# Kernel tuning notes

Measured on AMD Instinct MI355X. Metric: run time of the kernel, lower is better.

## Reference

```python
import jax, jax.numpy as jnp
import numpy as np

BATCH, IN, OUT = 4096, 4096, 4096

def setup_inputs() -> dict:
    key = jax.random.key(0)
    kx, kw, kb = jax.random.split(key, 3)
    x = jax.random.normal(kx, (BATCH, IN), dtype=jnp.float32)
    weights = jax.random.normal(kw, (OUT, IN), dtype=jnp.float32)
    beta = jax.random.normal(kb, (1,), dtype=jnp.float32)
    return {"x": x, "weights": weights, "beta": beta}

def reference(x, weights, beta):
    # original: sum over input dim of broadcast multiply == x @ W^T
    row_sum = jnp.einsum('bi,oi->bo', x, weights)  # [batch, output]
    return jax.nn.relu(1.0 - beta + row_sum)
```

## Files before the change

### kernel.cpp

```cpp
#include <hip/hip_runtime.h>
#include <hip/hip_bf16.h>
#include <cstdint>
#include <cstddef>

#define MDIM 4096
#define NDIM 4096
#define KDIM 4096

#define BM 128
#define BN 128
#define BK 64

typedef __bf16 bf16_t;
typedef bf16_t bf16x8 __attribute__((ext_vector_type(8)));
typedef float f32x4 __attribute__((ext_vector_type(4)));

#define GLDS16(gsrc, ldst)                                                   \
    __builtin_amdgcn_global_load_lds(                                        \
        (__attribute__((address_space(1))) void*)(gsrc),                     \
        (__attribute__((address_space(3))) void*)(ldst), 16, 0, 0)

__global__ void cvt_f32_to_bf16(const float* __restrict__ src,
                                bf16_t* __restrict__ dst, int n) {
    int idx = (blockIdx.x * blockDim.x + threadIdx.x) * 8;
    int stride = gridDim.x * blockDim.x * 8;
    for (int i = idx; i < n; i += stride) {
        const float4* s = reinterpret_cast<const float4*>(src + i);
        float4 a = s[0];
        float4 b = s[1];
        bf16x8 o;
        o[0] = (bf16_t)a.x; o[1] = (bf16_t)a.y;
        o[2] = (bf16_t)a.z; o[3] = (bf16_t)a.w;
        o[4] = (bf16_t)b.x; o[5] = (bf16_t)b.y;
        o[6] = (bf16_t)b.z; o[7] = (bf16_t)b.w;
        *reinterpret_cast<bf16x8*>(dst + i) = o;
    }
}

__global__ void gemm_bt_bf16(const bf16_t* __restrict__ A,
                             const bf16_t* __restrict__ B,
                             const float* __restrict__ beta,
                             float* __restrict__ out) {
    __shared__ __align__(16) bf16_t sA[BM * BK];
    __shared__ __align__(16) bf16_t sB[BN * BK];

    const int tid  = threadIdx.x;
    const int wid  = tid >> 6;
    const int lane = tid & 63;
    const int wr   = wid >> 1;
    const int wc   = wid & 1;
    const int lrow = lane & 15;
    const int kgrp = lane >> 4;

    const int brow = blockIdx.y * BM;
    const int bcol = blockIdx.x * BN;

    f32x4 acc[4][4];
#pragma unroll
    for (int i = 0; i < 4; ++i)
#pragma unroll
        for (int j = 0; j < 4; ++j)
            acc[i][j] = (f32x4){0.f, 0.f, 0.f, 0.f};

    const bf16_t* gA = A + (size_t)brow * KDIM;
    const bf16_t* gB = B + (size_t)bcol * KDIM;

    for (int kt = 0; kt < KDIM; kt += BK) {
#pragma unroll
        for (int i = 0; i < 4; ++i) {
            int g   = i * 256 + tid;
            int row = g >> 3;
            int col = (g & 7) << 3;
            GLDS16(gA + (size_t)row * KDIM + kt + col, sA + g * 8);
            GLDS16(gB + (size_t)row * KDIM + kt + col, sB + g * 8);
        }
        __syncthreads();

#pragma unroll
        for (int ko = 0; ko < 2; ++ko) {
            bf16x8 av[4], bv[4];
#pragma unroll
            for (int mi = 0; mi < 4; ++mi)
                av[mi] = *reinterpret_cast<const bf16x8*>(
                    &sA[(wr * 64 + mi * 16 + lrow) * BK + ko * 32 + kgrp * 8]);
#pragma unroll
            for (int ni = 0; ni < 4; ++ni)
                bv[ni] = *reinterpret_cast<const bf16x8*>(
                    &sB[(wc * 64 + ni * 16 + lrow) * BK + ko * 32 + kgrp * 8]);
#pragma unroll
            for (int mi = 0; mi < 4; ++mi)
#pragma unroll
                for (int ni = 0; ni < 4; ++ni)
                    acc[mi][ni] = __builtin_amdgcn_mfma_f32_16x16x32_bf16(
                        av[mi], bv[ni], acc[mi][ni], 0, 0, 0);
        }
        __syncthreads();
    }

    const float bias = 1.0f - beta[0];
    float* outp = out + (size_t)(brow + wr * 64) * NDIM + bcol + wc * 64;
#pragma unroll
    for (int mi = 0; mi < 4; ++mi) {
#pragma unroll
        for (int ni = 0; ni < 4; ++ni) {
#pragma unroll
            for (int j = 0; j < 4; ++j) {
                int r = mi * 16 + kgrp * 4 + j;
                int c = ni * 16 + lrow;
                float v = acc[mi][ni][j] + bias;
                outp[(size_t)r * NDIM + c] = fmaxf(v, 0.0f);
            }
        }
    }
}

__global__ void gemm_f32_fallback(const float* __restrict__ A,
                                  const float* __restrict__ B,
                                  const float* __restrict__ beta,
                                  float* __restrict__ out) {
    __shared__ float sA[16][17];
    __shared__ float sB[16][17];
    const int tx = threadIdx.x, ty = threadIdx.y;
    const int m = blockIdx.y * 16 + ty;
    const int n = blockIdx.x * 16 + tx;
    float acc = 0.f;
    for (int k0 = 0; k0 < KDIM; k0 += 16) {
        sA[ty][tx] = A[(size_t)m * KDIM + k0 + tx];
        sB[ty][tx] = B[(size_t)(blockIdx.x * 16 + ty) * KDIM + k0 + tx];
        __syncthreads();
#pragma unroll
        for (int k = 0; k < 16; ++k)
            acc += sA[ty][k] * sB[tx][k];
        __syncthreads();
    }
    float v = acc + 1.0f - beta[0];
    out[(size_t)m * NDIM + n] = fmaxf(v, 0.f);
}

extern "C" void kernel_launch(void* const* d_in, const int* in_sizes, int n_in,
                              void* d_out, int out_size, void* d_ws, size_t ws_size,
                              hipStream_t stream) {
    const float* x    = (const float*)d_in[0];
    const float* w    = (const float*)d_in[1];
    const float* beta = (const float*)d_in[2];
    float* out        = (float*)d_out;

    const size_t nelem = (size_t)MDIM * (size_t)KDIM;
    const size_t need  = 2 * nelem * sizeof(bf16_t);

    if (ws_size >= need) {
        bf16_t* xb = (bf16_t*)d_ws;
        bf16_t* wb = xb + nelem;
        cvt_f32_to_bf16<<<2048, 256, 0, stream>>>(x, xb, (int)nelem);
        cvt_f32_to_bf16<<<2048, 256, 0, stream>>>(w, wb, (int)nelem);
        dim3 grid(NDIM / BN, MDIM / BM);
        gemm_bt_bf16<<<grid, 256, 0, stream>>>(xb, wb, beta, out);
    } else {
        dim3 grid(NDIM / 16, MDIM / 16);
        gemm_f32_fallback<<<grid, dim3(16, 16), 0, stream>>>(x, w, beta, out);
    }
}
```

Before: 179.1 us.

## Rewrite bf16 GEMM as 256x256 double-buffered pipelined kernel with swizzled LDS

Replaces the 128x128 single-buffered GEMM with a 256x256-tile, 512-thread kernel that uses 128KB of dynamic LDS, double-buffered across K steps. Global-to-LDS loads for future tiles are interleaved with four MFMA quadrants per iteration, using fine-grained vmcnt waits, barriers and setprio. The LDS layout is XOR-swizzled to reduce bank conflicts, and block IDs are remapped for L2 locality. The aim is to hide memory latency and raise MFMA utilisation. In exchange it brings heavy register pressure, a grid of only 256 blocks (one per CU), and a complex synchronisation scheme that is easy to get wrong.

```diff
diff --git a/kernel.cpp b/kernel.cpp
--- a/kernel.cpp
+++ b/kernel.cpp
@@ -7,9 +7,10 @@
 #define NDIM 4096
 #define KDIM 4096
 
-#define BM 128
-#define BN 128
+#define BM 256
+#define BN 256
 #define BK 64
+#define NT (KDIM / BK)
 
 typedef __bf16 bf16_t;
 typedef bf16_t bf16x8 __attribute__((ext_vector_type(8)));
@@ -19,6 +20,13 @@
     __builtin_amdgcn_global_load_lds(                                        \
         (__attribute__((address_space(1))) void*)(gsrc),                     \
         (__attribute__((address_space(3))) void*)(ldst), 16, 0, 0)
+
+#define BAR()   __builtin_amdgcn_s_barrier()
+#define LGKM0() asm volatile("s_waitcnt lgkmcnt(0)" ::: "memory")
+#define VM4()   asm volatile("s_waitcnt vmcnt(4)" ::: "memory")
+#define VM0()   asm volatile("s_waitcnt vmcnt(0)" ::: "memory")
+
+__device__ __forceinline__ int swz(int q) { return q ^ (((q >> 9) & 1) << 5); }
 
 __global__ void cvt_f32_to_bf16(const float* __restrict__ src,
                                 bf16_t* __restrict__ dst, int n) {
@@ -37,81 +45,140 @@
     }
 }
 
-__global__ void gemm_bt_bf16(const bf16_t* __restrict__ A,
-                             const bf16_t* __restrict__ B,
-                             const float* __restrict__ beta,
-                             float* __restrict__ out) {
-    __shared__ __align__(16) bf16_t sA[BM * BK];
-    __shared__ __align__(16) bf16_t sB[BN * BK];
-
-    const int tid  = threadIdx.x;
-    const int wid  = tid >> 6;
-    const int lane = tid & 63;
-    const int wr   = wid >> 1;
-    const int wc   = wid & 1;
-    const int lrow = lane & 15;
-    const int kgrp = lane >> 4;
-
-    const int brow = blockIdx.y * BM;
-    const int bcol = blockIdx.x * BN;
-
-    f32x4 acc[4][4];
-#pragma unroll
-    for (int i = 0; i < 4; ++i)
+
+#define LOAD_A_HALF(MH, BUF) do {                                            \
+  _Pragma("unroll") for (int mi = 0; mi < 4; ++mi)                           \
+  _Pragma("unroll") for (int ko = 0; ko < 2; ++ko)                           \
+    av[mi][ko] = *(const bf16x8*)(ldsb + ((BUF) << 16) + a_off[(MH)*4 + mi][ko]); \
+} while (0)
+
+#define LOAD_B_PAIR(NH, BUF) do {                                            \
+  _Pragma("unroll") for (int ni = 0; ni < 2; ++ni)                           \
+  _Pragma("unroll") for (int ko = 0; ko < 2; ++ko)                           \
+    bv[(NH)*2 + ni][ko] = *(const bf16x8*)(ldsb + ((BUF) << 16) + b_off[(NH)*2 + ni][ko]); \
+} while (0)
+
+#define MFMA_QUAD(MH, NH) do {                                               \
+  _Pragma("unroll") for (int mi = 0; mi < 4; ++mi)                           \
+  _Pragma("unroll") for (int ni = 0; ni < 2; ++ni)                           \
+  _Pragma("unroll") for (int ko = 0; ko < 2; ++ko)                           \
+    acc[(MH)*4 + mi][(NH)*2 + ni] = __builtin_amdgcn_mfma_f32_16x16x32_bf16( \
+        av[mi][ko], bv[(NH)*2 + ni][ko], acc[(MH)*4 + mi][(NH)*2 + ni], 0, 0, 0); \
+} while (0)
+
+__global__ __launch_bounds__(512, 2) void gemm256(const bf16_t* __restrict__ A,
+                                                  const bf16_t* __restrict__ B,
+                                                  const float* __restrict__ beta,
+                                                  float* __restrict__ out) {
+    extern __shared__ char ldsb[];
+
+    const int tid    = threadIdx.x;
+    const int wid    = tid >> 6;
+    const int lane   = tid & 63;
+    const int warp_m = wid >> 2;
+    const int warp_n = wid & 3;
+    const int lrow   = lane & 15;
+    const int kgrp   = lane >> 4;
+
+    const int bid  = blockIdx.x;
+    const int sbid = (bid & 7) * 32 + (bid >> 3);
+    const int brow = (sbid >> 4) * BM;
+    const int bcol = (sbid & 15) * BN;
+
+    const int p0 = tid * 16, p1 = (tid + 512) * 16;
+    const int q0 = swz(p0), q1 = swz(p1);
+    const int rh0 = q0 >> 7, ce0 = (q0 & 127) >> 1;
+    const int rh1 = q1 >> 7, ce1 = (q1 & 127) >> 1;
+
+    const bf16_t* gA = A + (size_t)brow * KDIM;
+    const bf16_t* gB = B + (size_t)bcol * KDIM;
+
+    auto stageA = [&](int t, int h) {
+        const int slot = ((t & 1) << 16) | (h << 14);
+        GLDS16(gA + (size_t)(h * 128 + rh0) * KDIM + t * BK + ce0, ldsb + slot + p0);
+        GLDS16(gA + (size_t)(h * 128 + rh1) * KDIM + t * BK + ce1, ldsb + slot + p1);
+    };
+    auto stageB = [&](int t, int h) {
+        const int slot = ((t & 1) << 16) | ((2 + h) << 14);
+        GLDS16(gB + (size_t)(h * 128 + rh0) * KDIM + t * BK + ce0, ldsb + slot + p0);
+        GLDS16(gB + (size_t)(h * 128 + rh1) * KDIM + t * BK + ce1, ldsb + slot + p1);
+    };
+
+    int a_off[8][2];
+#pragma unroll
+    for (int mi = 0; mi < 8; ++mi)
+#pragma unroll
+        for (int ko = 0; ko < 2; ++ko)
+            a_off[mi][ko] = (warp_m << 14) +
+                swz((mi * 16 + lrow) * 128 + (ko * 32 + kgrp * 8) * 2);
+    int b_off[4][2];
+#pragma unroll
+    for (int ni = 0; ni < 4; ++ni)
+#pragma unroll
+        for (int ko = 0; ko < 2; ++ko)
+            b_off[ni][ko] = ((2 + (warp_n >> 1)) << 14) +
+                swz(((warp_n & 1) * 64 + ni * 16 + lrow) * 128 + (ko * 32 + kgrp * 8) * 2);
+
+    f32x4 acc[8][4];
+#pragma unroll
+    for (int i = 0; i < 8; ++i)
 #pragma unroll
         for (int j = 0; j < 4; ++j)
             acc[i][j] = (f32x4){0.f, 0.f, 0.f, 0.f};
 
-    const bf16_t* gA = A + (size_t)brow * KDIM;
-    const bf16_t* gB = B + (size_t)bcol * KDIM;
-
-    for (int kt = 0; kt < KDIM; kt += BK) {
-#pragma unroll
-        for (int i = 0; i < 4; ++i) {
-            int g   = i * 256 + tid;
-            int row = g >> 3;
-            int col = (g & 7) << 3;
-            GLDS16(gA + (size_t)row * KDIM + kt + col, sA + g * 8);
-            GLDS16(gB + (size_t)row * KDIM + kt + col, sB + g * 8);
-        }
-        __syncthreads();
-
-#pragma unroll
-        for (int ko = 0; ko < 2; ++ko) {
-            bf16x8 av[4], bv[4];
-#pragma unroll
-            for (int mi = 0; mi < 4; ++mi)
-                av[mi] = *reinterpret_cast<const bf16x8*>(
-                    &sA[(wr * 64 + mi * 16 + lrow) * BK + ko * 32 + kgrp * 8]);
-#pragma unroll
-            for (int ni = 0; ni < 4; ++ni)
-                bv[ni] = *reinterpret_cast<const bf16x8*>(
-                    &sB[(wc * 64 + ni * 16 + lrow) * BK + ko * 32 + kgrp * 8]);
-#pragma unroll
-            for (int mi = 0; mi < 4; ++mi)
-#pragma unroll
-                for (int ni = 0; ni < 4; ++ni)
-                    acc[mi][ni] = __builtin_amdgcn_mfma_f32_16x16x32_bf16(
-                        av[mi], bv[ni], acc[mi][ni], 0, 0, 0);
-        }
-        __syncthreads();
+    bf16x8 av[4][2];
+    bf16x8 bv[4][2];
+
+    stageA(0, 0); stageA(0, 1); stageB(0, 0); stageB(0, 1);
+    stageA(1, 0); stageB(1, 0);
+    VM4();
+    BAR();
+
+    for (int t = 0; t < NT; ++t) {
+        const int buf = t & 1;
+        LOAD_A_HALF(0, buf);
+        LOAD_B_PAIR(0, buf);
+        if (t + 1 < NT) stageA(t + 1, 1);
+        BAR(); LGKM0();
+        __builtin_amdgcn_s_setprio(1);
+        MFMA_QUAD(0, 0);
+        __builtin_amdgcn_s_setprio(0);
+        BAR();
+        LOAD_B_PAIR(1, buf);
+        if (t + 1 < NT) stageB(t + 1, 1);
+        BAR(); LGKM0();
+        __builtin_amdgcn_s_setprio(1);
+        MFMA_QUAD(0, 1);
+        __builtin_amdgcn_s_setprio(0);
+        BAR();
+        LOAD_A_HALF(1, buf);
+        if (t + 2 < NT) stageB(t + 2, 0);
+        BAR(); LGKM0();
+        __builtin_amdgcn_s_setprio(1);
+        MFMA_QUAD(1, 0);
+        __builtin_amdgcn_s_setprio(0);
+        BAR();
+        if (t + 2 < NT) stageA(t + 2, 0);
+        BAR(); LGKM0();
+        __builtin_amdgcn_s_setprio(1);
+        MFMA_QUAD(1, 1);
+        __builtin_amdgcn_s_setprio(0);
+        if (t < NT - 2) { VM4(); } else { VM0(); }
+        BAR();
     }
 
     const float bias = 1.0f - beta[0];
-    float* outp = out + (size_t)(brow + wr * 64) * NDIM + bcol + wc * 64;
-#pragma unroll
-    for (int mi = 0; mi < 4; ++mi) {
-#pragma unroll
-        for (int ni = 0; ni < 4; ++ni) {
+    float* outp = out + (size_t)(brow + warp_m * 128) * NDIM + bcol + warp_n * 64;
+#pragma unroll
+    for (int mi = 0; mi < 8; ++mi)
+#pragma unroll
+        for (int ni = 0; ni < 4; ++ni)
 #pragma unroll
             for (int j = 0; j < 4; ++j) {
-                int r = mi * 16 + kgrp * 4 + j;
-                int c = ni * 16 + lrow;
-                float v = acc[mi][ni][j] + bias;
-                outp[(size_t)r * NDIM + c] = fmaxf(v, 0.0f);
+                const int r = mi * 16 + kgrp * 4 + j;
+                const int c = ni * 16 + lrow;
+                outp[(size_t)r * NDIM + c] = fmaxf(acc[mi][ni][j] + bias, 0.0f);
             }
-        }
-    }
 }
 
 __global__ void gemm_f32_fallback(const float* __restrict__ A,
@@ -151,10 +218,11 @@
     if (ws_size >= need) {
         bf16_t* xb = (bf16_t*)d_ws;
         bf16_t* wb = xb + nelem;
+        hipFuncSetAttribute((const void*)gemm256,
+                            hipFuncAttributeMaxDynamicSharedMemorySize, 131072);
         cvt_f32_to_bf16<<<2048, 256, 0, stream>>>(x, xb, (int)nelem);
         cvt_f32_to_bf16<<<2048, 256, 0, stream>>>(w, wb, (int)nelem);
-        dim3 grid(NDIM / BN, MDIM / BM);
-        gemm_bt_bf16<<<grid, 256, 0, stream>>>(xb, wb, beta, out);
+        gemm256<<<256, 512, 131072, stream>>>(xb, wb, beta, out);
     } else {
         dim3 grid(NDIM / 16, MDIM / 16);
         gemm_f32_fallback<<<grid, dim3(16, 16), 0, stream>>>(x, w, beta, out);
```

After: 159.5 us. 10.9% less time.
